# Performance work log

Hardware: AMD Instinct MI355X
Metric: run time of the kernel (lower is better)

The kernel has to match this reference:

```python
import jax, jax.numpy as jnp
import numpy as np

TAU = 0.2
EPS = 1e-12  # matches torch F.normalize eps


def setup_inputs() -> dict:
    key = jax.random.key(0)
    k1, k2 = jax.random.split(key)
    N, D = 8192, 128
    h1 = jax.random.normal(k1, (N, D), dtype=jnp.float32)
    h2 = jax.random.normal(k2, (N, D), dtype=jnp.float32)
    return {"h1": h1, "h2": h2}


def _l2norm(x):
    # torch.nn.functional.normalize: x / max(||x||, eps)
    n = jnp.sqrt(jnp.sum(x * x, axis=1, keepdims=True))
    return x / jnp.maximum(n, EPS)


def _nt_xent(h1, h2):
    h1n = _l2norm(h1)
    h2n = _l2norm(h2)
    inter = jnp.exp((h1n @ h1n.T) / TAU)  # [N, N]
    intra = jnp.exp((h1n @ h2n.T) / TAU)  # [N, N]
    pos = jnp.diagonal(intra)
    neg = inter.sum(axis=1) + intra.sum(axis=1) - jnp.diagonal(inter)
    return -jnp.log(pos / neg)  # [N]


def reference(h1, h2):
    l1 = _nt_xent(h1, h2)
    l2 = _nt_xent(h2, h1)
    return jnp.mean((l1 + l2) * 0.5)
```

## Files before the change

### kernel.cpp

```cpp
#include <hip/hip_runtime.h>
#include <math.h>


constexpr int D = 128;
constexpr float E5 = 148.4131591025766f;

typedef __attribute__((ext_vector_type(16))) float f32x16;

__global__ __launch_bounds__(256) void normalize_kernel(
    const float2* __restrict__ h1, const float2* __restrict__ h2,
    unsigned short* __restrict__ g1b, unsigned short* __restrict__ g2b,
    float* __restrict__ d12, float* __restrict__ acc, float* __restrict__ out,
    int N)
{
    const float SC = sqrtf(5.0f * 1.44269504088896340736f);
    int gid = blockIdx.x * 256 + threadIdx.x;
    if (gid < 4 * N) acc[gid] = 0.f;
    if (gid == 0) out[0] = 0.f;

    int row  = blockIdx.x * 4 + (threadIdx.x >> 6);
    int lane = threadIdx.x & 63;
    float2 u = h1[(size_t)row * 64 + lane];
    float2 w = h2[(size_t)row * 64 + lane];
    float ss1 = u.x * u.x + u.y * u.y;
    float ss2 = w.x * w.x + w.y * w.y;
    float s12 = u.x * w.x + u.y * w.y;
#pragma unroll
    for (int off = 32; off > 0; off >>= 1) {
        ss1 += __shfl_xor(ss1, off, 64);
        ss2 += __shfl_xor(ss2, off, 64);
        s12 += __shfl_xor(s12, off, 64);
    }
    float n1 = fmaxf(sqrtf(ss1), 1e-12f);
    float n2 = fmaxf(sqrtf(ss2), 1e-12f);
    float c1 = SC / n1, c2 = SC / n2;
    int p1 = __builtin_amdgcn_cvt_pk_fp8_f32(u.x * c1, u.y * c1, 0, false);
    int p2 = __builtin_amdgcn_cvt_pk_fp8_f32(w.x * c2, w.y * c2, 0, false);
    g1b[(size_t)row * 64 + lane] = (unsigned short)(p1 & 0xffff);
    g2b[(size_t)row * 64 + lane] = (unsigned short)(p2 & 0xffff);
    if (lane == 0) d12[row] = 5.f * s12 / (n1 * n2);
}

__global__ __launch_bounds__(256, 2) void gram_mfma_kernel(
    const unsigned char* __restrict__ g1b, const unsigned char* __restrict__ g2b,
    float* __restrict__ r11, float* __restrict__ r12,
    float* __restrict__ c12, float* __restrict__ r22, int N)
{
    const int z = blockIdx.z;
    const bool SYM = (z != 1);
    const unsigned char* X; const unsigned char* Y; float* rrow;
    if (z == 0)      { X = g1b; Y = g1b; rrow = r11; }
    else if (z == 1) { X = g1b; Y = g2b; rrow = r12; }
    else             { X = g2b; Y = g2b; rrow = r22; }
    float* ctgt = SYM ? rrow : c12;

    const int iTile = blockIdx.x;
    int nT, dBase = 0;
    if (SYM) {
        if (blockIdx.y < 4)                     { nT = 8; dBase = blockIdx.y * 8; }
        else if (blockIdx.y == 4 && iTile < 32) { nT = 1; dBase = 32; }
        else return;
    } else {
        nT = 8;
    }

    __shared__ long Ys[128 * 16];

    const int tx   = threadIdx.x;
    const int lane = tx & 63;
    const int l32  = lane & 31, lhi = lane >> 5;
    const int wi   = (tx >> 6) >> 1, wj = (tx >> 6) & 1;
    const int iBase = iTile * 128;

    long a[2][8];
#pragma unroll
    for (int st = 0; st < 2; ++st) {
        const unsigned char* xp =
            X + (size_t)(iBase + wi * 64 + st * 32 + l32) * D + lhi * 8;
#pragma unroll
        for (int ks = 0; ks < 8; ++ks)
            a[st][ks] = *(const long*)(xp + ks * 16);
    }

    float racc0[16], racc1[16];
#pragma unroll
    for (int r = 0; r < 16; ++r) { racc0[r] = 0.f; racc1[r] = 0.f; }

    auto jTileOf = [&](int t) {
        return SYM ? ((iTile + dBase + t) & 63) : ((int)blockIdx.y * 8 + t);
    };

    long2 v[4];
    {
        const long2* yp = (const long2*)(Y + (size_t)jTileOf(0) * 128 * D);
#pragma unroll
        for (int i = 0; i < 4; ++i) v[i] = yp[i * 256 + tx];
    }

    const int j0 = wj * 64 + l32;
    const int j1 = j0 + 32;
    const int sw0 = j0 & 15, sw1 = j1 & 15;

    for (int t = 0; t < nT; ++t) {
        __syncthreads();
#pragma unroll
        for (int i = 0; i < 4; ++i) {
            int chunk = i * 256 + tx;
            int j = chunk >> 3, c = chunk & 7;
            int f0p = (2 * c) ^ (j & 15);
            int base = f0p & ~1;
            long2 w = v[i];
            if (j & 1) { long tmp = w.x; w.x = w.y; w.y = tmp; }
            *(long2*)&Ys[j * 16 + base] = w;
        }
        __syncthreads();

        if (t + 1 < nT) {
            const long2* yp = (const long2*)(Y + (size_t)jTileOf(t + 1) * 128 * D);
#pragma unroll
            for (int i = 0; i < 4; ++i) v[i] = yp[i * 256 + tx];
        }

        f32x16 acc00, acc01, acc10, acc11;
#pragma unroll
        for (int r = 0; r < 16; ++r) {
            acc00[r] = 0.f; acc01[r] = 0.f; acc10[r] = 0.f; acc11[r] = 0.f;
        }

#pragma unroll
        for (int ks = 0; ks < 8; ++ks) {
            int f = 2 * ks + lhi;
            long b0 = Ys[j0 * 16 + (f ^ sw0)];
            long b1 = Ys[j1 * 16 + (f ^ sw1)];
            acc00 = __builtin_amdgcn_mfma_f32_32x32x16_fp8_fp8(a[0][ks], b0, acc00, 0, 0, 0);
            acc10 = __builtin_amdgcn_mfma_f32_32x32x16_fp8_fp8(a[1][ks], b0, acc10, 0, 0, 0);
            acc01 = __builtin_amdgcn_mfma_f32_32x32x16_fp8_fp8(a[0][ks], b1, acc01, 0, 0, 0);
            acc11 = __builtin_amdgcn_mfma_f32_32x32x16_fp8_fp8(a[1][ks], b1, acc11, 0, 0, 0);
        }

        const bool doCols = !SYM || (dBase + t) != 0;
        if (doCols) {
            const int jBase = jTileOf(t) * 128;
            float cp0 = 0.f, cp1 = 0.f;
#pragma unroll
            for (int r = 0; r < 16; ++r) {
                float e00 = __builtin_amdgcn_exp2f(acc00[r]);
                float e01 = __builtin_amdgcn_exp2f(acc01[r]);
                float e10 = __builtin_amdgcn_exp2f(acc10[r]);
                float e11 = __builtin_amdgcn_exp2f(acc11[r]);
                racc0[r] += e00 + e01;
                racc1[r] += e10 + e11;
                cp0 += e00 + e10;
                cp1 += e01 + e11;
            }
            cp0 += __shfl_xor(cp0, 32, 64);
            cp1 += __shfl_xor(cp1, 32, 64);
            if (lane < 32) {
                atomicAdd(&ctgt[jBase + j0], cp0);
                atomicAdd(&ctgt[jBase + j1], cp1);
            }
        } else {
#pragma unroll
            for (int r = 0; r < 16; ++r) {
                racc0[r] += __builtin_amdgcn_exp2f(acc00[r]) +
                            __builtin_amdgcn_exp2f(acc01[r]);
                racc1[r] += __builtin_amdgcn_exp2f(acc10[r]) +
                            __builtin_amdgcn_exp2f(acc11[r]);
            }
        }
    }

#pragma unroll
    for (int r = 0; r < 16; ++r) {
        float s0 = racc0[r], s1 = racc1[r];
#pragma unroll
        for (int off = 1; off < 32; off <<= 1) {
            s0 += __shfl_xor(s0, off, 64);
            s1 += __shfl_xor(s1, off, 64);
        }
        if (l32 == 0) {
            int rowm = (r & 3) + 8 * (r >> 2) + 4 * lhi;
            atomicAdd(&rrow[iBase + wi * 64 + rowm], s0);
            atomicAdd(&rrow[iBase + wi * 64 + 32 + rowm], s1);
        }
    }
}

__global__ __launch_bounds__(256) void loss_reduce_kernel(
    const float* __restrict__ r11, const float* __restrict__ r12,
    const float* __restrict__ c12, const float* __restrict__ r22,
    const float* __restrict__ d12, float* __restrict__ out, int N)
{
    __shared__ float sm[256];
    float s = 0.f;
    for (int i = blockIdx.x * 256 + threadIdx.x; i < N; i += gridDim.x * 256) {
        float neg1 = r11[i] + r12[i] - E5;
        float neg2 = r22[i] + c12[i] - E5;
        s += 0.5f * (logf(neg1) + logf(neg2)) - d12[i];
    }
    sm[threadIdx.x] = s;
    __syncthreads();
    for (int w = 128; w > 0; w >>= 1) {
        if (threadIdx.x < w) sm[threadIdx.x] += sm[threadIdx.x + w];
        __syncthreads();
    }
    if (threadIdx.x == 0) atomicAdd(out, sm[0] / (float)N);
}

extern "C" void kernel_launch(void* const* d_in, const int* in_sizes, int n_in,
                              void* d_out, int out_size, void* d_ws, size_t ws_size,
                              hipStream_t stream) {
    const float* h1 = (const float*)d_in[0];
    const float* h2 = (const float*)d_in[1];
    const int N = in_sizes[0] / D;

    unsigned char* g1b = (unsigned char*)d_ws;
    unsigned char* g2b = g1b + (size_t)N * D;
    float* acc  = (float*)(g2b + (size_t)N * D);
    float* r11  = acc;
    float* r12  = acc + N;
    float* c12  = acc + 2 * N;
    float* r22  = acc + 3 * N;
    float* d12  = acc + 4 * N;
    float* out  = (float*)d_out;

    normalize_kernel<<<N / 4, 256, 0, stream>>>(
        (const float2*)h1, (const float2*)h2,
        (unsigned short*)g1b, (unsigned short*)g2b, d12, acc, out, N);

    dim3 grid(N / 128, 8, 3);
    gram_mfma_kernel<<<grid, 256, 0, stream>>>(g1b, g2b, r11, r12, c12, r22, N);

    loss_reduce_kernel<<<32, 256, 0, stream>>>(r11, r12, c12, r22, d12, out, N);
}
```

Measured before the change: 114.8 us.

## Double-buffer LDS tiles, halve per-block tile count, fuse final reduction via last-block counter

Gives each gram block four column tiles instead of eight, doubling the grid so more blocks are in flight. The shared-memory staging buffer is double-buffered, which removes one __syncthreads per tile. The separate loss-reduce kernel is dropped: a global atomic counter picks the last finishing block, which computes the log-sum loss and writes the output directly. This saves a kernel launch and tail, but adds more row atomics and a serial single-block reduction at the end. The useful-block count is hardcoded for N=8192.

After: 236.9 us. 106% more time.

```diff
diff --git a/kernel.cpp b/kernel.cpp
--- a/kernel.cpp
+++ b/kernel.cpp
@@ -10,13 +10,13 @@
 __global__ __launch_bounds__(256) void normalize_kernel(
     const float2* __restrict__ h1, const float2* __restrict__ h2,
     unsigned short* __restrict__ g1b, unsigned short* __restrict__ g2b,
-    float* __restrict__ d12, float* __restrict__ acc, float* __restrict__ out,
-    int N)
+    float* __restrict__ d12, float* __restrict__ acc,
+    unsigned* __restrict__ counter, int N)
 {
     const float SC = sqrtf(5.0f * 1.44269504088896340736f);
     int gid = blockIdx.x * 256 + threadIdx.x;
     if (gid < 4 * N) acc[gid] = 0.f;
-    if (gid == 0) out[0] = 0.f;
+    if (gid == 0) counter[0] = 0u;
 
     int row  = blockIdx.x * 4 + (threadIdx.x >> 6);
     int lane = threadIdx.x & 63;
@@ -44,7 +44,9 @@
 __global__ __launch_bounds__(256, 2) void gram_mfma_kernel(
     const unsigned char* __restrict__ g1b, const unsigned char* __restrict__ g2b,
     float* __restrict__ r11, float* __restrict__ r12,
-    float* __restrict__ c12, float* __restrict__ r22, int N)
+    float* __restrict__ c12, float* __restrict__ r22,
+    const float* __restrict__ d12, unsigned* __restrict__ counter,
+    float* __restrict__ out, int N, int totalUseful)
 {
     const int z = blockIdx.z;
     const bool SYM = (z != 1);
@@ -55,16 +57,18 @@
     float* ctgt = SYM ? rrow : c12;
 
     const int iTile = blockIdx.x;
-    int nT, dBase = 0;
+    int nT = 4, dBase = 0;
     if (SYM) {
-        if (blockIdx.y < 4)                     { nT = 8; dBase = blockIdx.y * 8; }
-        else if (blockIdx.y == 4 && iTile < 32) { nT = 1; dBase = 32; }
+        if (blockIdx.y < 8)                     { dBase = blockIdx.y * 4; }
+        else if (blockIdx.y == 8 && iTile < 32) { nT = 1; dBase = 32; }
         else return;
     } else {
-        nT = 8;
-    }
-
-    __shared__ long Ys[128 * 16];
+        if (blockIdx.y > 15) return;
+    }
+
+    __shared__ long Ys[2][128 * 16];
+    __shared__ float sm[256];
+    __shared__ int lastFlag;
 
     const int tx   = threadIdx.x;
     const int lane = tx & 63;
@@ -72,6 +76,10 @@
     const int wi   = (tx >> 6) >> 1, wj = (tx >> 6) & 1;
     const int iBase = iTile * 128;
 
+    auto jTileOf = [&](int t) {
+        return SYM ? ((iTile + dBase + t) & 63) : ((int)blockIdx.y * 4 + t);
+    };
+
     long a[2][8];
 #pragma unroll
     for (int st = 0; st < 2; ++st) {
@@ -86,10 +94,6 @@
 #pragma unroll
     for (int r = 0; r < 16; ++r) { racc0[r] = 0.f; racc1[r] = 0.f; }
 
-    auto jTileOf = [&](int t) {
-        return SYM ? ((iTile + dBase + t) & 63) : ((int)blockIdx.y * 8 + t);
-    };
-
     long2 v[4];
     {
         const long2* yp = (const long2*)(Y + (size_t)jTileOf(0) * 128 * D);
@@ -102,24 +106,22 @@
     const int sw0 = j0 & 15, sw1 = j1 & 15;
 
     for (int t = 0; t < nT; ++t) {
-        __syncthreads();
+        long* buf = Ys[t & 1];
 #pragma unroll
         for (int i = 0; i < 4; ++i) {
             int chunk = i * 256 + tx;
             int j = chunk >> 3, c = chunk & 7;
-            int f0p = (2 * c) ^ (j & 15);
-            int base = f0p & ~1;
+            int base = ((2 * c) ^ (j & 15)) & ~1;
             long2 w = v[i];
             if (j & 1) { long tmp = w.x; w.x = w.y; w.y = tmp; }
-            *(long2*)&Ys[j * 16 + base] = w;
-        }
-        __syncthreads();
-
+            *(long2*)&buf[j * 16 + base] = w;
+        }
         if (t + 1 < nT) {
             const long2* yp = (const long2*)(Y + (size_t)jTileOf(t + 1) * 128 * D);
 #pragma unroll
             for (int i = 0; i < 4; ++i) v[i] = yp[i * 256 + tx];
         }
+        __syncthreads();
 
         f32x16 acc00, acc01, acc10, acc11;
 #pragma unroll
@@ -130,8 +132,8 @@
 #pragma unroll
         for (int ks = 0; ks < 8; ++ks) {
             int f = 2 * ks + lhi;
-            long b0 = Ys[j0 * 16 + (f ^ sw0)];
-            long b1 = Ys[j1 * 16 + (f ^ sw1)];
+            long b0 = buf[j0 * 16 + (f ^ sw0)];
+            long b1 = buf[j1 * 16 + (f ^ sw1)];
             acc00 = __builtin_amdgcn_mfma_f32_32x32x16_fp8_fp8(a[0][ks], b0, acc00, 0, 0, 0);
             acc10 = __builtin_amdgcn_mfma_f32_32x32x16_fp8_fp8(a[1][ks], b0, acc10, 0, 0, 0);
             acc01 = __builtin_amdgcn_mfma_f32_32x32x16_fp8_fp8(a[0][ks], b1, acc01, 0, 0, 0);
@@ -184,27 +186,27 @@
             atomicAdd(&rrow[iBase + wi * 64 + 32 + rowm], s1);
         }
     }
-}
-
-__global__ __launch_bounds__(256) void loss_reduce_kernel(
-    const float* __restrict__ r11, const float* __restrict__ r12,
-    const float* __restrict__ c12, const float* __restrict__ r22,
-    const float* __restrict__ d12, float* __restrict__ out, int N)
-{
-    __shared__ float sm[256];
+
+    __threadfence();
+    if (tx == 0)
+        lastFlag = (atomicAdd(counter, 1u) == (unsigned)(totalUseful - 1));
+    __syncthreads();
+    if (!lastFlag) return;
+    __threadfence();
+
     float s = 0.f;
-    for (int i = blockIdx.x * 256 + threadIdx.x; i < N; i += gridDim.x * 256) {
-        float neg1 = r11[i] + r12[i] - E5;
-        float neg2 = r22[i] + c12[i] - E5;
+    for (int i = tx; i < N; i += 256) {
+        float neg1 = atomicAdd(&r11[i], 0.f) + atomicAdd(&r12[i], 0.f) - E5;
+        float neg2 = atomicAdd(&r22[i], 0.f) + atomicAdd(&c12[i], 0.f) - E5;
         s += 0.5f * (logf(neg1) + logf(neg2)) - d12[i];
     }
-    sm[threadIdx.x] = s;
+    sm[tx] = s;
     __syncthreads();
     for (int w = 128; w > 0; w >>= 1) {
-        if (threadIdx.x < w) sm[threadIdx.x] += sm[threadIdx.x + w];
+        if (tx < w) sm[tx] += sm[tx + w];
         __syncthreads();
     }
-    if (threadIdx.x == 0) atomicAdd(out, sm[0] / (float)N);
+    if (tx == 0) out[0] = sm[0] / (float)N;
 }
 
 extern "C" void kernel_launch(void* const* d_in, const int* in_sizes, int n_in,
@@ -222,14 +224,15 @@
     float* c12  = acc + 2 * N;
     float* r22  = acc + 3 * N;
     float* d12  = acc + 4 * N;
+    unsigned* counter = (unsigned*)(acc + 5 * N);
     float* out  = (float*)d_out;
 
     normalize_kernel<<<N / 4, 256, 0, stream>>>(
         (const float2*)h1, (const float2*)h2,
-        (unsigned short*)g1b, (unsigned short*)g2b, d12, acc, out, N);
-
-    dim3 grid(N / 128, 8, 3);
-    gram_mfma_kernel<<<grid, 256, 0, stream>>>(g1b, g2b, r11, r12, c12, r22, N);
-
-    loss_reduce_kernel<<<32, 256, 0, stream>>>(r11, r12, c12, r22, d12, out, N);
+        (unsigned short*)g1b, (unsigned short*)g2b, d12, acc, counter, N);
+
+    const int totalUseful = 544 * 2 + 1024;
+    dim3 grid(N / 128, 16, 3);
+    gram_mfma_kernel<<<grid, 256, 0, stream>>>(
+        g1b, g2b, r11, r12, c12, r22, d12, counter, out, N, totalUseful);
 }
```

## Split gram work into two-tile blocks with both tiles preloaded to LDS

Applied to the files above, without the earlier changes.

Each block now handles 2 column tiles instead of 8, so the grid grows from 8 to 32 blocks along y. Both tiles are loaded into a doubled LDS buffer up front with a single barrier, replacing the per-tile register-prefetch pipeline. Column-sum atomics are deferred until after the row reduction. This gives far more blocks to fill the GPU, at the cost of more A-fragment reloads, more row atomics per row, and double the LDS per block.

After: 137.5 us. 19.7% more time.

```diff
diff --git a/kernel.cpp b/kernel.cpp
--- a/kernel.cpp
+++ b/kernel.cpp
@@ -55,16 +55,14 @@
     float* ctgt = SYM ? rrow : c12;
 
     const int iTile = blockIdx.x;
-    int nT, dBase = 0;
+    int nT = 2, dBase = 0;
     if (SYM) {
-        if (blockIdx.y < 4)                     { nT = 8; dBase = blockIdx.y * 8; }
-        else if (blockIdx.y == 4 && iTile < 32) { nT = 1; dBase = 32; }
+        if (blockIdx.y < 16)                     { dBase = blockIdx.y * 2; }
+        else if (blockIdx.y == 16 && iTile < 32) { nT = 1; dBase = 32; }
         else return;
-    } else {
-        nT = 8;
-    }
-
-    __shared__ long Ys[128 * 16];
+    }
+
+    __shared__ long Ys[2 * 2048];
 
     const int tx   = threadIdx.x;
     const int lane = tx & 63;
@@ -72,6 +70,10 @@
     const int wi   = (tx >> 6) >> 1, wj = (tx >> 6) & 1;
     const int iBase = iTile * 128;
 
+    auto jTileOf = [&](int t) {
+        return SYM ? ((iTile + dBase + t) & 63) : (2 * (int)blockIdx.y + t);
+    };
+
     long a[2][8];
 #pragma unroll
     for (int st = 0; st < 2; ++st) {
@@ -82,44 +84,38 @@
             a[st][ks] = *(const long*)(xp + ks * 16);
     }
 
+    for (int t = 0; t < nT; ++t) {
+        const long2* yp = (const long2*)(Y + (size_t)jTileOf(t) * 128 * D);
+        long2 v[4];
+#pragma unroll
+        for (int i = 0; i < 4; ++i) v[i] = yp[i * 256 + tx];
+        long* buf = Ys + t * 2048;
+#pragma unroll
+        for (int i = 0; i < 4; ++i) {
+            int chunk = i * 256 + tx;
+            int j = chunk >> 3, c = chunk & 7;
+            int base = ((2 * c) ^ (j & 15)) & ~1;
+            long2 w = v[i];
+            if (j & 1) { long tmp = w.x; w.x = w.y; w.y = tmp; }
+            *(long2*)&buf[j * 16 + base] = w;
+        }
+    }
+    __syncthreads();
+
     float racc0[16], racc1[16];
 #pragma unroll
     for (int r = 0; r < 16; ++r) { racc0[r] = 0.f; racc1[r] = 0.f; }
-
-    auto jTileOf = [&](int t) {
-        return SYM ? ((iTile + dBase + t) & 63) : ((int)blockIdx.y * 8 + t);
-    };
-
-    long2 v[4];
-    {
-        const long2* yp = (const long2*)(Y + (size_t)jTileOf(0) * 128 * D);
-#pragma unroll
-        for (int i = 0; i < 4; ++i) v[i] = yp[i * 256 + tx];
-    }
 
     const int j0 = wj * 64 + l32;
     const int j1 = j0 + 32;
     const int sw0 = j0 & 15, sw1 = j1 & 15;
 
-    for (int t = 0; t < nT; ++t) {
-        __syncthreads();
-#pragma unroll
-        for (int i = 0; i < 4; ++i) {
-            int chunk = i * 256 + tx;
-            int j = chunk >> 3, c = chunk & 7;
-            int f0p = (2 * c) ^ (j & 15);
-            int base = f0p & ~1;
-            long2 w = v[i];
-            if (j & 1) { long tmp = w.x; w.x = w.y; w.y = tmp; }
-            *(long2*)&Ys[j * 16 + base] = w;
-        }
-        __syncthreads();
-
-        if (t + 1 < nT) {
-            const long2* yp = (const long2*)(Y + (size_t)jTileOf(t + 1) * 128 * D);
-#pragma unroll
-            for (int i = 0; i < 4; ++i) v[i] = yp[i * 256 + tx];
-        }
+    float cpA[2] = {0.f, 0.f}, cpB[2] = {0.f, 0.f};
+
+#pragma unroll
+    for (int t = 0; t < 2; ++t) {
+        if (t >= nT) break;
+        const long* buf = Ys + t * 2048;
 
         f32x16 acc00, acc01, acc10, acc11;
 #pragma unroll
@@ -130,44 +126,28 @@
 #pragma unroll
         for (int ks = 0; ks < 8; ++ks) {
             int f = 2 * ks + lhi;
-            long b0 = Ys[j0 * 16 + (f ^ sw0)];
-            long b1 = Ys[j1 * 16 + (f ^ sw1)];
+            long b0 = buf[j0 * 16 + (f ^ sw0)];
+            long b1 = buf[j1 * 16 + (f ^ sw1)];
             acc00 = __builtin_amdgcn_mfma_f32_32x32x16_fp8_fp8(a[0][ks], b0, acc00, 0, 0, 0);
             acc10 = __builtin_amdgcn_mfma_f32_32x32x16_fp8_fp8(a[1][ks], b0, acc10, 0, 0, 0);
             acc01 = __builtin_amdgcn_mfma_f32_32x32x16_fp8_fp8(a[0][ks], b1, acc01, 0, 0, 0);
             acc11 = __builtin_amdgcn_mfma_f32_32x32x16_fp8_fp8(a[1][ks], b1, acc11, 0, 0, 0);
         }
 
+        float c0 = 0.f, c1 = 0.f;
+#pragma unroll
+        for (int r = 0; r < 16; ++r) {
+            float e00 = __builtin_amdgcn_exp2f(acc00[r]);
+            float e01 = __builtin_amdgcn_exp2f(acc01[r]);
+            float e10 = __builtin_amdgcn_exp2f(acc10[r]);
+            float e11 = __builtin_amdgcn_exp2f(acc11[r]);
+            racc0[r] += e00 + e01;
+            racc1[r] += e10 + e11;
+            c0 += e00 + e10;
+            c1 += e01 + e11;
+        }
         const bool doCols = !SYM || (dBase + t) != 0;
-        if (doCols) {
-            const int jBase = jTileOf(t) * 128;
-            float cp0 = 0.f, cp1 = 0.f;
-#pragma unroll
-            for (int r = 0; r < 16; ++r) {
-                float e00 = __builtin_amdgcn_exp2f(acc00[r]);
-                float e01 = __builtin_amdgcn_exp2f(acc01[r]);
-                float e10 = __builtin_amdgcn_exp2f(acc10[r]);
-                float e11 = __builtin_amdgcn_exp2f(acc11[r]);
-                racc0[r] += e00 + e01;
-                racc1[r] += e10 + e11;
-                cp0 += e00 + e10;
-                cp1 += e01 + e11;
-            }
-            cp0 += __shfl_xor(cp0, 32, 64);
-            cp1 += __shfl_xor(cp1, 32, 64);
-            if (lane < 32) {
-                atomicAdd(&ctgt[jBase + j0], cp0);
-                atomicAdd(&ctgt[jBase + j1], cp1);
-            }
-        } else {
-#pragma unroll
-            for (int r = 0; r < 16; ++r) {
-                racc0[r] += __builtin_amdgcn_exp2f(acc00[r]) +
-                            __builtin_amdgcn_exp2f(acc01[r]);
-                racc1[r] += __builtin_amdgcn_exp2f(acc10[r]) +
-                            __builtin_amdgcn_exp2f(acc11[r]);
-            }
-        }
+        if (doCols) { cpA[t] = c0; cpB[t] = c1; }
     }
 
 #pragma unroll
@@ -182,6 +162,20 @@
             int rowm = (r & 3) + 8 * (r >> 2) + 4 * lhi;
             atomicAdd(&rrow[iBase + wi * 64 + rowm], s0);
             atomicAdd(&rrow[iBase + wi * 64 + 32 + rowm], s1);
+        }
+    }
+
+#pragma unroll
+    for (int t = 0; t < 2; ++t) {
+        if (t >= nT) break;
+        if (SYM && (dBase + t) == 0) continue;
+        float c0 = cpA[t], c1 = cpB[t];
+        c0 += __shfl_xor(c0, 32, 64);
+        c1 += __shfl_xor(c1, 32, 64);
+        if (lane < 32) {
+            int jb = jTileOf(t) * 128;
+            atomicAdd(&ctgt[jb + j0], c0);
+            atomicAdd(&ctgt[jb + j1], c1);
         }
     }
 }
@@ -228,7 +222,7 @@
         (const float2*)h1, (const float2*)h2,
         (unsigned short*)g1b, (unsigned short*)g2b, d12, acc, out, N);
 
-    dim3 grid(N / 128, 8, 3);
+    dim3 grid(N / 128, 32, 3);
     gram_mfma_kernel<<<grid, 256, 0, stream>>>(g1b, g2b, r11, r12, c12, r22, N);
 
     loss_reduce_kernel<<<32, 256, 0, stream>>>(r11, r12, c12, r22, d12, out, N);
```
